# Optimization experiments

Hardware: AMD Instinct MI355X
Metric: run time of the kernel (lower is better)

The kernel has to match this reference:

```python
import jax, jax.numpy as jnp
import numpy as np

H = 8      # n_heads
E = 128    # d_keys (== D; required by out_projection Linear(D*n_heads, D))


def setup_inputs() -> dict:
    key = jax.random.key(0)
    ks = jax.random.split(key, 11)
    B, T, D = 64, 256, 128
    s = 0.02
    return {
        "x": jax.random.normal(ks[0], (B, T, D), dtype=jnp.float32),
        "Wq": jax.random.normal(ks[1], (D, H * E), dtype=jnp.float32) * s,
        "bq": jax.random.normal(ks[2], (H * E,), dtype=jnp.float32) * s,
        "Wk": jax.random.normal(ks[3], (D, H * E), dtype=jnp.float32) * s,
        "bk": jax.random.normal(ks[4], (H * E,), dtype=jnp.float32) * s,
        "Wv": jax.random.normal(ks[5], (D, H * E), dtype=jnp.float32) * s,
        "bv": jax.random.normal(ks[6], (H * E,), dtype=jnp.float32) * s,
        "Ws": jax.random.normal(ks[7], (T, 1), dtype=jnp.float32) * s,
        "bs": jax.random.normal(ks[8], (1,), dtype=jnp.float32) * s,
        "Wo": jax.random.normal(ks[9], (H * E, D), dtype=jnp.float32) * s,
        "bo": jax.random.normal(ks[10], (D,), dtype=jnp.float32) * s,
    }


def reference(x, Wq, bq, Wk, bk, Wv, bv, Ws, bs, Wo, bo):
    B, T, D = x.shape
    # Q/K/V projections -> [B, T, H, E]
    Q = (x @ Wq + bq).reshape(B, T, H, E)
    K = (x @ Wk + bk).reshape(B, T, H, E)
    V = (x @ Wv + bv).reshape(B, T, H, E)
    scale = 1.0 / jnp.sqrt(jnp.float32(E))
    # QK^T scores over time: [B, H, T, T] (query t, key j)
    scores = jnp.einsum('bthd,bjhd->bhtj', Q, K)
    # summary projection contracts the key axis j: T -> 1  => [B, H, T, 1]
    summary = (scale * scores) @ Ws + bs
    # softmax over the query axis t (dim=-2)
    beta = jax.nn.softmax(summary, axis=-2)[..., 0]        # [B, H, T]
    # weight V per (b, t, h) and sum over time -> [B, H, E]
    beta_cal = jnp.transpose(beta, (0, 2, 1))[..., None]   # [B, T, H, 1]
    result = jnp.sum(V * beta_cal, axis=1)                 # [B, H, E]
    out = result.reshape(B, H * E) @ Wo + bo               # [B, D]
    return out
```

## Files before the change

kernel.cpp:

```cpp
#include <hip/hip_runtime.h>
#include <hip/hip_bf16.h>


#define SCALE 0.08838834764831845f
#define MAGIC 0x13579BDFu
#define BAR() __asm__ volatile("s_waitcnt lgkmcnt(0)\n\ts_barrier" ::: "memory")

__global__ __launch_bounds__(256, 2)
void ta_one(const float* __restrict__ x,  const float* __restrict__ Wq,
            const float* __restrict__ Wk, const float* __restrict__ bk,
            const float* __restrict__ Wv, const float* __restrict__ bv,
            const float* __restrict__ Wsv,
            const float* __restrict__ Wo, const float* __restrict__ bov,
            float* __restrict__ ws, float* __restrict__ out)
{
    __shared__ __align__(16) float buf[8224];
    __shared__ __align__(16) float pB[1024];
    __shared__ __align__(16) float wsS[256];
    __shared__ __align__(16) float xwS[128];
    __shared__ __align__(16) float kwS[128];
    __shared__ __align__(16) float wqkS[128];
    __shared__ __align__(16) float betaS[256];
    __shared__ __align__(16) float xbS[128];
    __shared__ __align__(16) float resS[128];
    __shared__ float smx[4], sms[4];
    __shared__ float swS;

    const int tid = threadIdx.x;
    const int b = blockIdx.x, h = blockIdx.y;
    const int w = tid >> 6, l = tid & 63;
    const int q  = tid & 31, tc = tid >> 5;
    const int c8 = tid & 7,  r8 = tid >> 3;
    const float* xp0 = x + (size_t)b * 32768;

    float4 rx[32];
    #pragma unroll
    for (int j = 0; j < 32; ++j)
        rx[j] = ((const float4*)(xp0 + (size_t)(tc * 32 + j) * 128))[q];
    const float bkv = bk[h * 128 + (tid & 127)];
    const float bvv = bv[h * 128 + (tid & 127)];
    if (tid < 64) *(float4*)(wsS + 4 * tid) = *(const float4*)(Wsv + 4 * tid);
    BAR();

    {
        float4 acc = {0.f, 0.f, 0.f, 0.f};
        #pragma unroll
        for (int j = 0; j < 32; ++j) {
            const float s = wsS[tc * 32 + j];
            acc.x += s * rx[j].x; acc.y += s * rx[j].y;
            acc.z += s * rx[j].z; acc.w += s * rx[j].w;
        }
        *(float4*)(buf + tc * 128 + 4 * q) = acc;
    }
    BAR();
    if (tid < 128) {
        float v = 0.f;
        #pragma unroll
        for (int g = 0; g < 8; ++g) v += buf[g * 128 + tid];
        xwS[tid] = v;
    } else if (tid < 192) {
        float v = wsS[l] + wsS[l + 64] + wsS[l + 128] + wsS[l + 192];
        #pragma unroll
        for (int off = 32; off; off >>= 1) v += __shfl_xor(v, off, 64);
        if (l == 0) swS = v;
    }
    BAR();

    {
        float4 acc = {0.f, 0.f, 0.f, 0.f};
        #pragma unroll
        for (int j = 0; j < 16; ++j) {
            const int k = tc * 16 + j;
            const float4 wv = ((const float4*)(Wk + (size_t)k * 1024 + h * 128))[q];
            const float xv = xwS[k];
            acc.x += xv * wv.x; acc.y += xv * wv.y;
            acc.z += xv * wv.z; acc.w += xv * wv.w;
        }
        *(float4*)(pB + tc * 128 + 4 * q) = acc;
    }
    BAR();
    if (tid < 128) {
        float v = swS * bkv;
        #pragma unroll
        for (int g = 0; g < 8; ++g) v += pB[g * 128 + tid];
        kwS[tid] = v;
    }
    BAR();

    {
        #pragma unroll
        for (int rr = 0; rr < 4; ++rr) {
            const int o = 32 * rr + r8;
            const float* base = Wq + (size_t)o * 1024 + h * 128;
            float a = 0.f;
            #pragma unroll
            for (int m = 0; m < 4; ++m) {
                const int j4 = c8 + 8 * m;
                const float4 wv = *(const float4*)(base + 4 * j4);
                const float4 kv = *(const float4*)(kwS + 4 * j4);
                a += wv.x * kv.x + wv.y * kv.y + wv.z * kv.z + wv.w * kv.w;
            }
            buf[c8 * 257 + o] = a;
        }
    }
    BAR();
    if (tid < 128) {
        float v = 0.f;
        #pragma unroll
        for (int g = 0; g < 8; ++g) v += buf[g * 257 + tid];
        wqkS[tid] = v * SCALE;
    }
    BAR();

    {
        const float4 qv = ((const float4*)wqkS)[q];
        #pragma unroll
        for (int j = 0; j < 32; ++j) {
            const float s = rx[j].x * qv.x + rx[j].y * qv.y
                          + rx[j].z * qv.z + rx[j].w * qv.w;
            buf[q * 257 + tc * 32 + j] = s;
        }
    }
    BAR();

    {
        float v = 0.f;
        #pragma unroll
        for (int g = 0; g < 32; ++g) v += buf[g * 257 + tid];
        float m = v;
        #pragma unroll
        for (int off = 32; off; off >>= 1) m = fmaxf(m, __shfl_xor(m, off, 64));
        if (l == 0) smx[w] = m;
        BAR();
        const float M = fmaxf(fmaxf(smx[0], smx[1]), fmaxf(smx[2], smx[3]));
        const float e = __expf(v - M);
        float ssum = e;
        #pragma unroll
        for (int off = 32; off; off >>= 1) ssum += __shfl_xor(ssum, off, 64);
        if (l == 0) sms[w] = ssum;
        BAR();
        betaS[tid] = e / (sms[0] + sms[1] + sms[2] + sms[3]);
    }
    BAR();

    {
        float4 acc = {0.f, 0.f, 0.f, 0.f};
        #pragma unroll
        for (int j = 0; j < 32; ++j) {
            const float bb = betaS[tc * 32 + j];
            acc.x += bb * rx[j].x; acc.y += bb * rx[j].y;
            acc.z += bb * rx[j].z; acc.w += bb * rx[j].w;
        }
        *(float4*)(buf + tc * 128 + 4 * q) = acc;
    }
    BAR();
    if (tid < 128) {
        float v = 0.f;
        #pragma unroll
        for (int g = 0; g < 8; ++g) v += buf[g * 128 + tid];
        xbS[tid] = v;
    }
    BAR();

    {
        float4 acc = {0.f, 0.f, 0.f, 0.f};
        #pragma unroll
        for (int j = 0; j < 16; ++j) {
            const int dd = tc * 16 + j;
            const float4 wv = ((const float4*)(Wv + (size_t)dd * 1024 + h * 128))[q];
            const float xv = xbS[dd];
            acc.x += xv * wv.x; acc.y += xv * wv.y;
            acc.z += xv * wv.z; acc.w += xv * wv.w;
        }
        *(float4*)(pB + tc * 128 + 4 * q) = acc;
    }
    BAR();
    if (tid < 128) {
        float v = bvv;
        #pragma unroll
        for (int g = 0; g < 8; ++g) v += pB[g * 128 + tid];
        resS[tid] = v;
    }
    BAR();

    {
        float4 acc = {0.f, 0.f, 0.f, 0.f};
        #pragma unroll
        for (int j = 0; j < 16; ++j) {
            const int e = tc * 16 + j;
            const float4 wv = ((const float4*)(Wo + (size_t)(h * 128 + e) * 128))[q];
            const float rv = resS[e];
            acc.x += rv * wv.x; acc.y += rv * wv.y;
            acc.z += rv * wv.z; acc.w += rv * wv.w;
        }
        *(float4*)(buf + tc * 128 + 4 * q) = acc;
    }
    __syncthreads();

    float* part = ws;
    unsigned* flags = (unsigned*)(ws + 65536);
    if (h < 7) {
        if (tid < 128) {
            float v = 0.f;
            #pragma unroll
            for (int g = 0; g < 8; ++g) v += buf[g * 128 + tid];
            part[(size_t)(b * 8 + h) * 128 + tid] = v;
            __threadfence();
        }
        __syncthreads();
        if (tid == 0) atomicExch(&flags[b * 8 + h], MAGIC);
    } else {
        if (tid == 0) {
            #pragma unroll
            for (int i = 0; i < 7; ++i)
                while (atomicCAS(&flags[b * 8 + i], MAGIC, MAGIC) != MAGIC) {}
        }
        __syncthreads();
        if (tid < 128) {
            float v = bov[tid];
            #pragma unroll
            for (int g = 0; g < 8; ++g) v += buf[g * 128 + tid];
            #pragma unroll
            for (int i = 0; i < 7; ++i)
                v += atomicAdd(&part[(size_t)(b * 8 + i) * 128 + tid], 0.f);
            out[(size_t)b * 128 + tid] = v;
        }
    }
}

extern "C" void kernel_launch(void* const* d_in, const int* in_sizes, int n_in,
                              void* d_out, int out_size, void* d_ws, size_t ws_size,
                              hipStream_t stream) {
    const float* x  = (const float*)d_in[0];
    const float* Wq = (const float*)d_in[1];
    const float* Wk = (const float*)d_in[3];
    const float* bk = (const float*)d_in[4];
    const float* Wv = (const float*)d_in[5];
    const float* bv = (const float*)d_in[6];
    const float* Ws = (const float*)d_in[7];
    const float* Wo = (const float*)d_in[9];
    const float* bo = (const float*)d_in[10];
    float* out = (float*)d_out;
    float* ws  = (float*)d_ws;

    ta_one<<<dim3(64, 8), dim3(256), 0, stream>>>(x, Wq, Wk, bk, Wv, bv, Ws, Wo, bo, ws, out);
}
```

Baseline: 109.8 us.

## Drop register-cached x tile; re-read x from global and shrink shared buffers

The 32 float4 registers per thread that held the x tile are removed, and x is re-read from global memory (likely L2-resident) in each of the three passes that use it. The scores pass is restructured to a row-dot layout with an 8-way reduction instead of a 32-way one. Shared memory shrinks from about 37KB to about 8KB because the large buf and pB are merged into one small buffer. This cuts register and LDS pressure so more blocks can be resident, at the cost of reading x three times from global memory instead of once.

```diff
diff --git a/kernel.cpp b/kernel.cpp
--- a/kernel.cpp
+++ b/kernel.cpp
@@ -14,8 +14,7 @@
             const float* __restrict__ Wo, const float* __restrict__ bov,
             float* __restrict__ ws, float* __restrict__ out)
 {
-    __shared__ __align__(16) float buf[8224];
-    __shared__ __align__(16) float pB[1024];
+    __shared__ __align__(16) float buf[2056];
     __shared__ __align__(16) float wsS[256];
     __shared__ __align__(16) float xwS[128];
     __shared__ __align__(16) float kwS[128];
@@ -29,14 +28,10 @@
     const int tid = threadIdx.x;
     const int b = blockIdx.x, h = blockIdx.y;
     const int w = tid >> 6, l = tid & 63;
-    const int q  = tid & 31, tc = tid >> 5;
+    const int q5 = tid & 31, tc = tid >> 5;
     const int c8 = tid & 7,  r8 = tid >> 3;
     const float* xp0 = x + (size_t)b * 32768;
 
-    float4 rx[32];
-    #pragma unroll
-    for (int j = 0; j < 32; ++j)
-        rx[j] = ((const float4*)(xp0 + (size_t)(tc * 32 + j) * 128))[q];
     const float bkv = bk[h * 128 + (tid & 127)];
     const float bvv = bv[h * 128 + (tid & 127)];
     if (tid < 64) *(float4*)(wsS + 4 * tid) = *(const float4*)(Wsv + 4 * tid);
@@ -44,13 +39,14 @@
 
     {
         float4 acc = {0.f, 0.f, 0.f, 0.f};
-        #pragma unroll
+        const float4* xp = (const float4*)(xp0 + (size_t)(tc * 32) * 128) + q5;
+        #pragma unroll 8
         for (int j = 0; j < 32; ++j) {
+            const float4 v = xp[(size_t)j * 32];
             const float s = wsS[tc * 32 + j];
-            acc.x += s * rx[j].x; acc.y += s * rx[j].y;
-            acc.z += s * rx[j].z; acc.w += s * rx[j].w;
-        }
-        *(float4*)(buf + tc * 128 + 4 * q) = acc;
+            acc.x += s * v.x; acc.y += s * v.y; acc.z += s * v.z; acc.w += s * v.w;
+        }
+        *(float4*)(buf + tc * 128 + 4 * q5) = acc;
     }
     BAR();
     if (tid < 128) {
@@ -68,21 +64,21 @@
 
     {
         float4 acc = {0.f, 0.f, 0.f, 0.f};
+        const float4* wp = (const float4*)(Wk + (size_t)(tc * 16) * 1024 + h * 128) + q5;
         #pragma unroll
         for (int j = 0; j < 16; ++j) {
-            const int k = tc * 16 + j;
-            const float4 wv = ((const float4*)(Wk + (size_t)k * 1024 + h * 128))[q];
-            const float xv = xwS[k];
+            const float4 wv = wp[(size_t)j * 256];
+            const float xv = xwS[tc * 16 + j];
             acc.x += xv * wv.x; acc.y += xv * wv.y;
             acc.z += xv * wv.z; acc.w += xv * wv.w;
         }
-        *(float4*)(pB + tc * 128 + 4 * q) = acc;
+        *(float4*)(buf + tc * 128 + 4 * q5) = acc;
     }
     BAR();
     if (tid < 128) {
         float v = swS * bkv;
         #pragma unroll
-        for (int g = 0; g < 8; ++g) v += pB[g * 128 + tid];
+        for (int g = 0; g < 8; ++g) v += buf[g * 128 + tid];
         kwS[tid] = v;
     }
     BAR();
@@ -90,8 +86,8 @@
     {
         #pragma unroll
         for (int rr = 0; rr < 4; ++rr) {
-            const int o = 32 * rr + r8;
-            const float* base = Wq + (size_t)o * 1024 + h * 128;
+            const int d = 32 * rr + r8;
+            const float* base = Wq + (size_t)d * 1024 + h * 128;
             float a = 0.f;
             #pragma unroll
             for (int m = 0; m < 4; ++m) {
@@ -100,7 +96,7 @@
                 const float4 kv = *(const float4*)(kwS + 4 * j4);
                 a += wv.x * kv.x + wv.y * kv.y + wv.z * kv.z + wv.w * kv.w;
             }
-            buf[c8 * 257 + o] = a;
+            buf[c8 * 257 + d] = a;
         }
     }
     BAR();
@@ -113,20 +109,27 @@
     BAR();
 
     {
-        const float4 qv = ((const float4*)wqkS)[q];
-        #pragma unroll
-        for (int j = 0; j < 32; ++j) {
-            const float s = rx[j].x * qv.x + rx[j].y * qv.y
-                          + rx[j].z * qv.z + rx[j].w * qv.w;
-            buf[q * 257 + tc * 32 + j] = s;
-        }
-    }
-    BAR();
-
-    {
-        float v = 0.f;
-        #pragma unroll
-        for (int g = 0; g < 32; ++g) v += buf[g * 257 + tid];
+        #pragma unroll
+        for (int rr = 0; rr < 8; ++rr) {
+            const int t = 32 * rr + r8;
+            const float* base = xp0 + (size_t)t * 128;
+            float a = 0.f;
+            #pragma unroll
+            for (int m = 0; m < 4; ++m) {
+                const int j4 = c8 + 8 * m;
+                const float4 xv = *(const float4*)(base + 4 * j4);
+                const float4 qv = *(const float4*)(wqkS + 4 * j4);
+                a += xv.x * qv.x + xv.y * qv.y + xv.z * qv.z + xv.w * qv.w;
+            }
+            buf[c8 * 257 + t] = a;
+        }
+    }
+    BAR();
+
+    {
+        float v = 0.f;
+        #pragma unroll
+        for (int g = 0; g < 8; ++g) v += buf[g * 257 + tid];
         float m = v;
         #pragma unroll
         for (int off = 32; off; off >>= 1) m = fmaxf(m, __shfl_xor(m, off, 64));
@@ -145,13 +148,14 @@
 
     {
         float4 acc = {0.f, 0.f, 0.f, 0.f};
-        #pragma unroll
+        const float4* xp = (const float4*)(xp0 + (size_t)(tc * 32) * 128) + q5;
+        #pragma unroll 8
         for (int j = 0; j < 32; ++j) {
+            const float4 v = xp[(size_t)j * 32];
             const float bb = betaS[tc * 32 + j];
-            acc.x += bb * rx[j].x; acc.y += bb * rx[j].y;
-            acc.z += bb * rx[j].z; acc.w += bb * rx[j].w;
-        }
-        *(float4*)(buf + tc * 128 + 4 * q) = acc;
+            acc.x += bb * v.x; acc.y += bb * v.y; acc.z += bb * v.z; acc.w += bb * v.w;
+        }
+        *(float4*)(buf + tc * 128 + 4 * q5) = acc;
     }
     BAR();
     if (tid < 128) {
@@ -164,36 +168,36 @@
 
     {
         float4 acc = {0.f, 0.f, 0.f, 0.f};
+        const float4* wp = (const float4*)(Wv + (size_t)(tc * 16) * 1024 + h * 128) + q5;
         #pragma unroll
         for (int j = 0; j < 16; ++j) {
-            const int dd = tc * 16 + j;
-            const float4 wv = ((const float4*)(Wv + (size_t)dd * 1024 + h * 128))[q];
-            const float xv = xbS[dd];
+            const float4 wv = wp[(size_t)j * 256];
+            const float xv = xbS[tc * 16 + j];
             acc.x += xv * wv.x; acc.y += xv * wv.y;
             acc.z += xv * wv.z; acc.w += xv * wv.w;
         }
-        *(float4*)(pB + tc * 128 + 4 * q) = acc;
+        *(float4*)(buf + tc * 128 + 4 * q5) = acc;
     }
     BAR();
     if (tid < 128) {
         float v = bvv;
         #pragma unroll
-        for (int g = 0; g < 8; ++g) v += pB[g * 128 + tid];
+        for (int g = 0; g < 8; ++g) v += buf[g * 128 + tid];
         resS[tid] = v;
     }
     BAR();
 
     {
         float4 acc = {0.f, 0.f, 0.f, 0.f};
+        const float4* wp = (const float4*)(Wo + (size_t)(h * 128 + tc * 16) * 128) + q5;
         #pragma unroll
         for (int j = 0; j < 16; ++j) {
-            const int e = tc * 16 + j;
-            const float4 wv = ((const float4*)(Wo + (size_t)(h * 128 + e) * 128))[q];
-            const float rv = resS[e];
+            const float4 wv = wp[(size_t)j * 32];
+            const float rv = resS[tc * 16 + j];
             acc.x += rv * wv.x; acc.y += rv * wv.y;
             acc.z += rv * wv.z; acc.w += rv * wv.w;
         }
-        *(float4*)(buf + tc * 128 + 4 * q) = acc;
+        *(float4*)(buf + tc * 128 + 4 * q5) = acc;
     }
     __syncthreads();
 
```

Result: slower. 112.1 us (+2.1%).
